# Performance work log

Hardware: AMD Instinct MI355X
Metric: run time of the kernel (lower is better)

The kernel has to match this reference:

```python
import jax, jax.numpy as jnp
import numpy as np

DN = ('NCH', 'OIH', 'NCH')  # conv dimension numbers: [batch, channel, length]

def setup_inputs() -> dict:
    key = jax.random.key(0)
    ks = jax.random.split(key, 8)
    B, S, L, D, F, V = 16, 64, 128, 512, 256, 30000
    return {
        'text': jax.random.randint(ks[0], (B, S, L), 0, V),
        'embed': jax.random.normal(ks[1], (V, D), dtype=jnp.float32),
        'w3': jax.random.normal(ks[2], (F, D, 3), dtype=jnp.float32) * 0.05,
        'b3': jax.random.normal(ks[3], (F,), dtype=jnp.float32) * 0.05,
        'w4': jax.random.normal(ks[4], (F, D, 4), dtype=jnp.float32) * 0.05,
        'b4': jax.random.normal(ks[5], (F,), dtype=jnp.float32) * 0.05,
        'w5': jax.random.normal(ks[6], (F, D, 5), dtype=jnp.float32) * 0.05,
        'b5': jax.random.normal(ks[7], (F,), dtype=jnp.float32) * 0.05,
    }

def reference(text, embed, w3, b3, w4, b4, w5, b5):
    B, S, L = text.shape
    # Embed tokens, flatten episodes x utterances into one batch, channels-first.
    x = embed[text]                                   # [B, S, L, D]
    x = x.reshape(B * S, L, -1).transpose(0, 2, 1)    # [BS, D, L]
    outs = []
    for w, b in ((w3, b3), (w4, b4), (w5, b5)):
        y = jax.lax.conv_general_dilated(x, w, (1,), 'VALID', dimension_numbers=DN)
        # max-over-time pooling (valid conv -> length L-K+1)
        outs.append(jnp.max(y + b[None, :, None], axis=2))  # [BS, F]
    out = jax.nn.relu(jnp.concatenate(outs, axis=1))  # [BS, 3F]
    return out.reshape(B, S, -1)
```

## Files before the change

### kernel.cpp

```cpp
#include <hip/hip_runtime.h>
#include <hip/hip_bf16.h>


typedef __bf16 bf16x8 __attribute__((ext_vector_type(8)));
typedef float f32x4 __attribute__((ext_vector_type(4)));

#define XROWS 132
#define XELEMS ((size_t)1024 * XROWS * 512)
#define SLAB_STRIDE 520
#define SLAB_ROWS 133
#define SLAB_BYTES (SLAB_ROWS * SLAB_STRIDE * 2)
#define WQ_ELEMS 1572864

__device__ __forceinline__ void async16(const void* g, void* l) {
    __builtin_amdgcn_global_load_lds(
        (const __attribute__((address_space(1))) void*)g,
        (__attribute__((address_space(3))) void*)l, 16, 0, 0);
}

__global__ void pack_x_kernel(const int* __restrict__ text,
                              const float* __restrict__ embed,
                              __bf16* __restrict__ x) {
    const int tid  = threadIdx.x;
    const int rr   = blockIdx.x * 4 + (tid >> 6);
    const int lane = tid & 63;
    const int bs   = rr / XROWS;
    const int t    = rr - bs * XROWS;
    __bf16* dst = x + (size_t)rr * 512 + lane * 8;
    bf16x8 o = {};
    if (t < 128) {
        const int token = text[bs * 128 + t];
        const float* src = embed + (size_t)token * 512 + lane * 8;
        const float4 v0 = *(const float4*)(src);
        const float4 v1 = *(const float4*)(src + 4);
        o[0] = (__bf16)v0.x; o[1] = (__bf16)v0.y;
        o[2] = (__bf16)v0.z; o[3] = (__bf16)v0.w;
        o[4] = (__bf16)v1.x; o[5] = (__bf16)v1.y;
        o[6] = (__bf16)v1.z; o[7] = (__bf16)v1.w;
    }
    *(bf16x8*)dst = o;
}

__global__ void pack_w_kernel(const float* __restrict__ w3,
                              const float* __restrict__ w4,
                              const float* __restrict__ w5,
                              __bf16* __restrict__ wq) {
    const int t    = blockIdx.x * 256 + threadIdx.x;
    const int g    = t >> 6;
    const int lane = t & 63;
    int rel, Kw; const float* w;
    if (g < 768)       { rel = g;        Kw = 3; w = w3; }
    else if (g < 1792) { rel = g - 768;  Kw = 4; w = w4; }
    else               { rel = g - 1792; Kw = 5; w = w5; }
    const int kq  = rel >> 4;
    const int n16 = rel & 15;
    const int f   = n16 * 16 + (lane & 15);
    const int k0  = kq * 32 + (lane >> 4) * 8;
    const int tap = k0 >> 9;
    const int d0  = k0 & 511;
    const float* src = w + ((size_t)f * 512 + d0) * Kw + tap;
    bf16x8 o;
#pragma unroll
    for (int j = 0; j < 8; ++j) o[j] = (__bf16)src[j * Kw];
    *(bf16x8*)(wq + (size_t)t * 8) = o;
}

__global__ __launch_bounds__(512, 2) void conv_gemm_kernel(
        const __bf16* __restrict__ x,
        const __bf16* __restrict__ wq,
        const float* __restrict__ b3,
        const float* __restrict__ b4,
        const float* __restrict__ b5,
        float* __restrict__ out) {
    extern __shared__ __bf16 slab[];

    const int tid  = threadIdx.x;
    const int wave = tid >> 6;
    const int lane = tid & 63;

    const int lin = blockIdx.x;
    const int xcd = lin & 7;
    const int idx = lin >> 3;
    const int bsh = idx / 3;
    const int c   = idx - bsh * 3;
    const int bs  = bsh * 8 + xcd;
    const int KW  = 3 + c;
    const int nkq = KW << 4;
    const int cbase = (c == 0) ? 0 : (c == 1) ? 393216 : 917504;

    const __bf16* xb = x + (size_t)bs * (XROWS * 512);

    for (int r = wave; r < XROWS; r += 8)
        async16(xb + r * 512 + lane * 8, &slab[r * SLAB_STRIDE]);
    __syncthreads();

    const int wm = wave & 1, wn = wave >> 1;
    const int lm = lane & 15, lk = lane >> 4;

    const __bf16* ap = slab + (wm * 64 + lm) * SLAB_STRIDE + lk * 8;
    const __bf16* bp = wq + cbase + (size_t)(wn * 4) * 512 + lane * 8;

    f32x4 acc[4][4];
#pragma unroll
    for (int i = 0; i < 4; ++i)
#pragma unroll
        for (int j = 0; j < 4; ++j) acc[i][j] = (f32x4){0.f, 0.f, 0.f, 0.f};

    bf16x8 A2[2][4], B4[4][4];

    auto loadB = [&](bf16x8* d, int kb) {
        const __bf16* p = bp + (size_t)kb * 8192;
        d[0] = *(const bf16x8*)(p);
        d[1] = *(const bf16x8*)(p + 512);
        d[2] = *(const bf16x8*)(p + 1024);
        d[3] = *(const bf16x8*)(p + 1536);
    };
    auto mfma16 = [&](const bf16x8* a, const bf16x8* b) {
#pragma unroll
        for (int mt = 0; mt < 4; ++mt)
#pragma unroll
            for (int nt = 0; nt < 4; ++nt)
                acc[mt][nt] = __builtin_amdgcn_mfma_f32_16x16x32_bf16(
                    a[mt], b[nt], acc[mt][nt], 0, 0, 0);
    };

    loadB(B4[0], 0); loadB(B4[1], 1); loadB(B4[2], 2); loadB(B4[3], 3);
#pragma unroll
    for (int mt = 0; mt < 4; ++mt) {
        A2[0][mt] = *(const bf16x8*)(ap + mt * (16 * SLAB_STRIDE));
        A2[1][mt] = *(const bf16x8*)(ap + 32 + mt * (16 * SLAB_STRIDE));
    }

    for (int tap = 0; tap < KW; ++tap) {
        const int kq0 = tap << 4;
#pragma unroll
        for (int q = 0; q < 16; ++q) {
            mfma16(A2[q & 1], B4[q & 3]);
            {
                const int off = (q + 2 < 16) ? (q + 2) * 32
                                             : SLAB_STRIDE + (q - 14) * 32;
#pragma unroll
                for (int mt = 0; mt < 4; ++mt)
                    A2[q & 1][mt] = *(const bf16x8*)
                        (ap + off + mt * (16 * SLAB_STRIDE));
            }
            {
                int kb = kq0 + q + 4;
                kb = (kb < nkq) ? kb : (nkq - 1);
                loadB(B4[q & 3], kb);
            }
        }
        ap += SLAB_STRIDE;
    }

    const int Tv = 126 - c;
    float cmax[4];
#pragma unroll
    for (int nt = 0; nt < 4; ++nt) {
        float mx = -3.0e38f;
#pragma unroll
        for (int mt = 0; mt < 4; ++mt) {
            const int mb = wm * 64 + mt * 16 + lk * 4;
#pragma unroll
            for (int r = 0; r < 4; ++r) {
                const float v = acc[mt][nt][r];
                if (mb + r < Tv) mx = fmaxf(mx, v);
            }
        }
        mx = fmaxf(mx, __shfl_xor(mx, 16, 64));
        mx = fmaxf(mx, __shfl_xor(mx, 32, 64));
        cmax[nt] = mx;
    }
    __syncthreads();
    float* red = (float*)slab;
    if (lk == 0) {
#pragma unroll
        for (int nt = 0; nt < 4; ++nt)
            red[wm * 256 + wn * 64 + nt * 16 + lm] = cmax[nt];
    }
    __syncthreads();
    if (tid < 256) {
        const float* bias = (c == 0) ? b3 : (c == 1) ? b4 : b5;
        float v = fmaxf(red[tid], red[256 + tid]) + bias[tid];
        out[(size_t)bs * 768 + c * 256 + tid] = fmaxf(v, 0.f);
    }
}

extern "C" void kernel_launch(void* const* d_in, const int* in_sizes, int n_in,
                              void* d_out, int out_size, void* d_ws, size_t ws_size,
                              hipStream_t stream) {
    const int*   text  = (const int*)d_in[0];
    const float* embed = (const float*)d_in[1];
    const float* w3    = (const float*)d_in[2];
    const float* b3    = (const float*)d_in[3];
    const float* w4    = (const float*)d_in[4];
    const float* b4    = (const float*)d_in[5];
    const float* w5    = (const float*)d_in[6];
    const float* b5    = (const float*)d_in[7];
    float* out = (float*)d_out;

    __bf16* x  = (__bf16*)d_ws;
    __bf16* wq = x + XELEMS;

    (void)hipFuncSetAttribute((const void*)conv_gemm_kernel,
                              hipFuncAttributeMaxDynamicSharedMemorySize,
                              SLAB_BYTES);

    pack_x_kernel<<<1024 * XROWS / 4, 256, 0, stream>>>(text, embed, x);
    pack_w_kernel<<<768, 256, 0, stream>>>(w3, w4, w5, wq);
    conv_gemm_kernel<<<3072, 512, SLAB_BYTES, stream>>>(x, wq, b3, b4, b5, out);
}
```

Before: 506.8 us.

## Use 16 waves per block with smaller per-wave tiles and scheduled interleaving

Doubles the block to 1024 threads, splitting M across 4 waves instead of 2 so each wave holds a 32x64 accumulator tile. B prefetch depth drops from 4 to 2, and sched_group_barrier hints interleave LDS reads, global loads and MFMAs. The aim is to cut register pressure and raise waves per CU to better hide load latency. In exchange each wave reloads the same B fragments, which doubles global/L2 traffic for weights per block, and the final reduction now combines four partial maxima.

```diff
diff --git a/kernel.cpp b/kernel.cpp
--- a/kernel.cpp
+++ b/kernel.cpp
@@ -65,7 +65,7 @@
     *(bf16x8*)(wq + (size_t)t * 8) = o;
 }
 
-__global__ __launch_bounds__(512, 2) void conv_gemm_kernel(
+__global__ __launch_bounds__(1024, 4) void conv_gemm_kernel(
         const __bf16* __restrict__ x,
         const __bf16* __restrict__ wq,
         const float* __restrict__ b3,
@@ -90,23 +90,23 @@
 
     const __bf16* xb = x + (size_t)bs * (XROWS * 512);
 
-    for (int r = wave; r < XROWS; r += 8)
+    for (int r = wave; r < XROWS; r += 16)
         async16(xb + r * 512 + lane * 8, &slab[r * SLAB_STRIDE]);
     __syncthreads();
 
-    const int wm = wave & 1, wn = wave >> 1;
+    const int wm = wave & 3, wn = wave >> 2;
     const int lm = lane & 15, lk = lane >> 4;
 
-    const __bf16* ap = slab + (wm * 64 + lm) * SLAB_STRIDE + lk * 8;
+    const __bf16* ap = slab + (wm * 32 + lm) * SLAB_STRIDE + lk * 8;
     const __bf16* bp = wq + cbase + (size_t)(wn * 4) * 512 + lane * 8;
 
-    f32x4 acc[4][4];
-#pragma unroll
-    for (int i = 0; i < 4; ++i)
+    f32x4 acc[2][4];
+#pragma unroll
+    for (int i = 0; i < 2; ++i)
 #pragma unroll
         for (int j = 0; j < 4; ++j) acc[i][j] = (f32x4){0.f, 0.f, 0.f, 0.f};
 
-    bf16x8 A2[2][4], B4[4][4];
+    bf16x8 A2[2][2], B2[2][4];
 
     auto loadB = [&](bf16x8* d, int kb) {
         const __bf16* p = bp + (size_t)kb * 8192;
@@ -115,40 +115,41 @@
         d[2] = *(const bf16x8*)(p + 1024);
         d[3] = *(const bf16x8*)(p + 1536);
     };
-    auto mfma16 = [&](const bf16x8* a, const bf16x8* b) {
-#pragma unroll
-        for (int mt = 0; mt < 4; ++mt)
+    auto loadA = [&](bf16x8* d, int off) {
+        d[0] = *(const bf16x8*)(ap + off);
+        d[1] = *(const bf16x8*)(ap + off + 16 * SLAB_STRIDE);
+    };
+    auto mfma8 = [&](const bf16x8* a, const bf16x8* b) {
+#pragma unroll
+        for (int mt = 0; mt < 2; ++mt)
 #pragma unroll
             for (int nt = 0; nt < 4; ++nt)
                 acc[mt][nt] = __builtin_amdgcn_mfma_f32_16x16x32_bf16(
                     a[mt], b[nt], acc[mt][nt], 0, 0, 0);
     };
 
-    loadB(B4[0], 0); loadB(B4[1], 1); loadB(B4[2], 2); loadB(B4[3], 3);
-#pragma unroll
-    for (int mt = 0; mt < 4; ++mt) {
-        A2[0][mt] = *(const bf16x8*)(ap + mt * (16 * SLAB_STRIDE));
-        A2[1][mt] = *(const bf16x8*)(ap + 32 + mt * (16 * SLAB_STRIDE));
-    }
+    loadA(A2[0], 0);  loadA(A2[1], 32);
+    loadB(B2[0], 0);  loadB(B2[1], 1);
 
     for (int tap = 0; tap < KW; ++tap) {
         const int kq0 = tap << 4;
 #pragma unroll
         for (int q = 0; q < 16; ++q) {
-            mfma16(A2[q & 1], B4[q & 3]);
-            {
-                const int off = (q + 2 < 16) ? (q + 2) * 32
-                                             : SLAB_STRIDE + (q - 14) * 32;
-#pragma unroll
-                for (int mt = 0; mt < 4; ++mt)
-                    A2[q & 1][mt] = *(const bf16x8*)
-                        (ap + off + mt * (16 * SLAB_STRIDE));
-            }
-            {
-                int kb = kq0 + q + 4;
-                kb = (kb < nkq) ? kb : (nkq - 1);
-                loadB(B4[q & 3], kb);
-            }
+            mfma8(A2[q & 1], B2[q & 1]);
+            const int off = (q + 2 < 16) ? (q + 2) * 32
+                                         : SLAB_STRIDE + (q - 14) * 32;
+            loadA(A2[q & 1], off);
+            int kb = kq0 + q + 2;
+            kb = (kb < nkq) ? kb : (nkq - 1);
+            loadB(B2[q & 1], kb);
+            __builtin_amdgcn_sched_group_barrier(0x020, 2, 0);
+            __builtin_amdgcn_sched_group_barrier(0x008, 2, 0);
+            __builtin_amdgcn_sched_group_barrier(0x100, 1, 0);
+            __builtin_amdgcn_sched_group_barrier(0x008, 2, 0);
+            __builtin_amdgcn_sched_group_barrier(0x020, 2, 0);
+            __builtin_amdgcn_sched_group_barrier(0x008, 2, 0);
+            __builtin_amdgcn_sched_group_barrier(0x100, 1, 0);
+            __builtin_amdgcn_sched_group_barrier(0x008, 2, 0);
         }
         ap += SLAB_STRIDE;
     }
@@ -159,8 +160,8 @@
     for (int nt = 0; nt < 4; ++nt) {
         float mx = -3.0e38f;
 #pragma unroll
-        for (int mt = 0; mt < 4; ++mt) {
-            const int mb = wm * 64 + mt * 16 + lk * 4;
+        for (int mt = 0; mt < 2; ++mt) {
+            const int mb = wm * 32 + mt * 16 + lk * 4;
 #pragma unroll
             for (int r = 0; r < 4; ++r) {
                 const float v = acc[mt][nt][r];
@@ -181,7 +182,8 @@
     __syncthreads();
     if (tid < 256) {
         const float* bias = (c == 0) ? b3 : (c == 1) ? b4 : b5;
-        float v = fmaxf(red[tid], red[256 + tid]) + bias[tid];
+        float v = fmaxf(fmaxf(red[tid], red[256 + tid]),
+                        fmaxf(red[512 + tid], red[768 + tid])) + bias[tid];
         out[(size_t)bs * 768 + c * 256 + tid] = fmaxf(v, 0.f);
     }
 }
@@ -208,5 +210,5 @@
 
     pack_x_kernel<<<1024 * XROWS / 4, 256, 0, stream>>>(text, embed, x);
     pack_w_kernel<<<768, 256, 0, stream>>>(w3, w4, w5, wq);
-    conv_gemm_kernel<<<3072, 512, SLAB_BYTES, stream>>>(x, wq, b3, b4, b5, out);
-}
+    conv_gemm_kernel<<<3072, 1024, SLAB_BYTES, stream>>>(x, wq, b3, b4, b5, out);
+}
```

Measured after the change: 590.6 us. 16.5% more time.
